# Optimization experiments

Measured on AMD Instinct MI355X. Metric: run time of the kernel, lower is better.

## Reference

```python
import jax, jax.numpy as jnp
import numpy as np

N_NODES = 8_000_000
N_GRAPHS = 16384
OUT_DIM = 256
LABEL_MAX = 300  # some labels >= OUT_DIM to exercise the bounds check


def setup_inputs() -> dict:
    key = jax.random.key(0)
    k1, k2 = jax.random.split(key)
    x = jax.random.randint(k1, (N_NODES,), 0, LABEL_MAX, dtype=jnp.int32)
    # ptr: sorted segment boundaries with ptr[0]=0, ptr[-1]=N_NODES
    inner = jnp.sort(jax.random.randint(k2, (N_GRAPHS - 1,), 0, N_NODES, dtype=jnp.int32))
    ptr = jnp.concatenate([jnp.zeros((1,), jnp.int32), inner,
                           jnp.full((1,), N_NODES, jnp.int32)])
    node_weights = jnp.ones((N_NODES,), jnp.float32)  # all-ones -> plain counting
    return {"x": x, "ptr": ptr, "node_weights": node_weights,
            "num_graphs": N_GRAPHS, "out_dim": OUT_DIM}


def reference(x, ptr, node_weights, num_graphs, out_dim):
    # Segmented histogram: out[g, c] = # nodes in graph g with label c (c < out_dim).
    n = x.shape[0]
    # graph id of each node from CSR ptr boundaries
    seg = jnp.searchsorted(ptr, jnp.arange(n, dtype=ptr.dtype), side="right") - 1
    valid = x < out_dim
    xc = jnp.where(valid, x, 0)                 # clamp out-of-range labels
    w = jnp.where(valid, node_weights, 0.0)     # mask them out of the count
    out = jnp.zeros((num_graphs, out_dim), jnp.float32).at[seg, xc].add(w)
    return out
```

## Files before the change

kernel.cpp:

```cpp
#include <hip/hip_runtime.h>


extern "C" __global__ void seg_hist_kernel(const int* __restrict__ x,
                                           const int* __restrict__ ptr,
                                           const float* __restrict__ w,
                                           float* __restrict__ out,
                                           int out_dim) {
    extern __shared__ float hist[];

    const int g = blockIdx.x;
    const int start = ptr[g];
    const int end = ptr[g + 1];

    for (int c = threadIdx.x; c < out_dim; c += blockDim.x) hist[c] = 0.0f;
    __syncthreads();

    for (int i = start + (int)threadIdx.x; i < end; i += (int)blockDim.x) {
        const int lbl = x[i];
        if ((unsigned)lbl < (unsigned)out_dim) {
            atomicAdd(&hist[lbl], w[i]);
        }
    }
    __syncthreads();

    float* o = out + (size_t)g * (size_t)out_dim;
    for (int c = threadIdx.x; c < out_dim; c += blockDim.x) o[c] = hist[c];
}

extern "C" void kernel_launch(void* const* d_in, const int* in_sizes, int n_in,
                              void* d_out, int out_size, void* d_ws, size_t ws_size,
                              hipStream_t stream) {
    const int* x   = (const int*)d_in[0];
    const int* ptr = (const int*)d_in[1];
    const float* w = (const float*)d_in[2];
    float* out     = (float*)d_out;

    const int num_graphs = in_sizes[1] - 1;
    const int out_dim    = out_size / num_graphs;

    dim3 grid(num_graphs);
    dim3 block(256);
    size_t lds_bytes = (size_t)out_dim * sizeof(float);

    seg_hist_kernel<<<grid, block, lds_bytes, stream>>>(x, ptr, w, out, out_dim);
}
```

Baseline: 52.05 us.

## Assign one wavefront per graph with per-wave LDS histograms and vectorized loads

Replaces the one-block-per-graph kernel with a kernel where each 64-lane wavefront owns a graph and its own 256-bin LDS histogram, removing block-wide barriers. Interior elements are read with int4/float4 loads after peeling unaligned head and tail elements. A grid-stride loop over graphs and a fixed output dimension allow unrolled zeroing and writeback. Each graph now gets only 64 lanes, so long segments may cause load imbalance; a fallback kernel keeps other output dimensions working.

```diff
diff --git a/kernel.cpp b/kernel.cpp
--- a/kernel.cpp
+++ b/kernel.cpp
@@ -1,30 +1,78 @@
 #include <hip/hip_runtime.h>
 
 
-extern "C" __global__ void seg_hist_kernel(const int* __restrict__ x,
-                                           const int* __restrict__ ptr,
-                                           const float* __restrict__ w,
-                                           float* __restrict__ out,
-                                           int out_dim) {
-    extern __shared__ float hist[];
+#define ODIM 256
 
+extern "C" __global__ __launch_bounds__(256, 8)
+void wave_hist_kernel(const int* __restrict__ x, const int* __restrict__ ptr,
+                      const float* __restrict__ w, float* __restrict__ out,
+                      int num_graphs) {
+    __shared__ float hist[4][ODIM];
+
+    const int wv   = (int)threadIdx.x >> 6;
+    const int lane = (int)threadIdx.x & 63;
+    float* h = hist[wv];
+
+    const int total_waves = (int)gridDim.x * 4;
+
+    for (int g = (int)blockIdx.x * 4 + wv; g < num_graphs; g += total_waves) {
+        const int s = ptr[g];
+        const int e = ptr[g + 1];
+
+        #pragma unroll
+        for (int k = 0; k < 4; ++k) h[lane + (k << 6)] = 0.0f;
+
+        const int a0 = min((s + 3) & ~3, e);
+        const int a1 = max(e & ~3, a0);
+
+        {
+            const int i = s + lane;
+            if (i < a0) {
+                const int lbl = x[i];
+                if ((unsigned)lbl < (unsigned)ODIM) atomicAdd(&h[lbl], w[i]);
+            }
+        }
+
+        for (int i = a0 + lane * 4; i < a1; i += 64 * 4) {
+            const int4   l4 = *reinterpret_cast<const int4*>(x + i);
+            const float4 w4 = *reinterpret_cast<const float4*>(w + i);
+            if ((unsigned)l4.x < (unsigned)ODIM) atomicAdd(&h[l4.x], w4.x);
+            if ((unsigned)l4.y < (unsigned)ODIM) atomicAdd(&h[l4.y], w4.y);
+            if ((unsigned)l4.z < (unsigned)ODIM) atomicAdd(&h[l4.z], w4.z);
+            if ((unsigned)l4.w < (unsigned)ODIM) atomicAdd(&h[l4.w], w4.w);
+        }
+
+        {
+            const int i = a1 + lane;
+            if (i < e) {
+                const int lbl = x[i];
+                if ((unsigned)lbl < (unsigned)ODIM) atomicAdd(&h[lbl], w[i]);
+            }
+        }
+
+        float* row = out + (size_t)g * ODIM;
+        #pragma unroll
+        for (int k = 0; k < 4; ++k) row[lane + (k << 6)] = h[lane + (k << 6)];
+    }
+}
+
+extern "C" __global__ __launch_bounds__(256)
+void seg_hist_fallback(const int* __restrict__ x, const int* __restrict__ ptr,
+                       const float* __restrict__ w, float* __restrict__ out,
+                       int out_dim) {
+    extern __shared__ float fhist[];
     const int g = blockIdx.x;
     const int start = ptr[g];
     const int end = ptr[g + 1];
-
-    for (int c = threadIdx.x; c < out_dim; c += blockDim.x) hist[c] = 0.0f;
+    for (int c = (int)threadIdx.x; c < out_dim; c += 256) fhist[c] = 0.0f;
     __syncthreads();
-
-    for (int i = start + (int)threadIdx.x; i < end; i += (int)blockDim.x) {
+    for (int i = start + (int)threadIdx.x; i < end; i += 256) {
         const int lbl = x[i];
-        if ((unsigned)lbl < (unsigned)out_dim) {
-            atomicAdd(&hist[lbl], w[i]);
-        }
+        if ((unsigned)lbl < (unsigned)out_dim) atomicAdd(&fhist[lbl], w[i]);
     }
     __syncthreads();
-
     float* o = out + (size_t)g * (size_t)out_dim;
-    for (int c = threadIdx.x; c < out_dim; c += blockDim.x) o[c] = hist[c];
+    for (int c = (int)threadIdx.x; c < out_dim; c += 256) o[c] = fhist[c];
 }
 
 extern "C" void kernel_launch(void* const* d_in, const int* in_sizes, int n_in,
@@ -38,9 +86,12 @@
     const int num_graphs = in_sizes[1] - 1;
     const int out_dim    = out_size / num_graphs;
 
-    dim3 grid(num_graphs);
-    dim3 block(256);
-    size_t lds_bytes = (size_t)out_dim * sizeof(float);
+    if (out_dim != ODIM) {
+        seg_hist_fallback<<<num_graphs, 256, (size_t)out_dim * sizeof(float), stream>>>(
+            x, ptr, w, out, out_dim);
+        return;
+    }
 
-    seg_hist_kernel<<<grid, block, lds_bytes, stream>>>(x, ptr, w, out, out_dim);
+    const int n_blocks = (num_graphs + 3) / 4;
+    wave_hist_kernel<<<n_blocks, 256, 0, stream>>>(x, ptr, w, out, num_graphs);
 }
```

After: 52.68 us. No clear change (+1.2%).
